# Kernel optimization log

Measured on AMD Instinct MI355X. Metric: run time of the kernel, lower is better.

## Reference

```python
import jax, jax.numpy as jnp
import numpy as np

N_NODES = 20000
N_EDGES = 50000
IN_DIM = 128
HID = 128
OUT_DIM = 64
N_PAIRS = 128
N_LAYERS = 2
N_HEADS = 4


def setup_inputs() -> dict:
    key = jax.random.key(0)
    ks = jax.random.split(key, 32)
    s = 0.05
    def p(k, shape):
        return jax.random.normal(k, shape, jnp.float32) * s
    inp = {}
    inp["node_features"] = jax.random.normal(ks[0], (N_NODES, IN_DIM), jnp.float32)
    inp["edge_index"] = jax.random.randint(ks[1], (2, N_EDGES), 0, N_NODES, jnp.int32)
    inp["edge_timestamps"] = jax.random.uniform(ks[2], (N_EDGES,), jnp.float32)
    inp["target_pairs"] = jax.random.randint(ks[3], (N_PAIRS, 2), 0, N_NODES, jnp.int32)
    inp["in_W"] = p(ks[4], (HID, IN_DIM)); inp["in_b"] = p(ks[5], (HID,))
    inp["te_W1"] = p(ks[6], (N_LAYERS, HID, 1)); inp["te_b1"] = p(ks[7], (N_LAYERS, HID))
    inp["te_W2"] = p(ks[8], (N_LAYERS, HID, HID)); inp["te_b2"] = p(ks[9], (N_LAYERS, HID))
    inp["attn_in_W"] = p(ks[10], (N_LAYERS, 3 * HID, HID)); inp["attn_in_b"] = p(ks[11], (N_LAYERS, 3 * HID))
    inp["attn_out_W"] = p(ks[12], (N_LAYERS, HID, HID)); inp["attn_out_b"] = p(ks[13], (N_LAYERS, HID))
    inp["ft_W"] = p(ks[14], (N_LAYERS, HID, HID)); inp["ft_b"] = p(ks[15], (N_LAYERS, HID))
    inp["op_W"] = p(ks[16], (N_LAYERS, HID, HID)); inp["op_b"] = p(ks[17], (N_LAYERS, HID))
    inp["out1_W"] = p(ks[18], (HID, HID)); inp["out1_b"] = p(ks[19], (HID,))
    inp["out2_W"] = p(ks[20], (OUT_DIM, HID)); inp["out2_b"] = p(ks[21], (OUT_DIM,))
    inp["lp1_W"] = p(ks[22], (HID, 2 * OUT_DIM)); inp["lp1_b"] = p(ks[23], (HID,))
    inp["lp2_W"] = p(ks[24], (HID // 2, HID)); inp["lp2_b"] = p(ks[25], (HID // 2,))
    inp["lp3_W"] = p(ks[26], (1, HID // 2)); inp["lp3_b"] = p(ks[27], (1,))
    return inp


def _forward(node_features, edge_index, edge_timestamps, target_pairs,
             in_W, in_b, te_W1, te_b1, te_W2, te_b2,
             attn_in_W, attn_in_b, attn_out_W, attn_out_b,
             ft_W, ft_b, op_W, op_b,
             out1_W, out1_b, out2_W, out2_b,
             lp1_W, lp1_b, lp2_W, lp2_b, lp3_W, lp3_b):
    N = node_features.shape[0]
    h = in_W.shape[0]
    H = N_HEADS
    d = h // H
    scale = 1.0 / np.sqrt(d).astype(np.float32)
    src, dst = edge_index[0], edge_index[1]
    # flattened target nodes; duplicates compute identical rows so dedup (torch.unique) is unneeded
    targets = target_pairs.reshape(-1)  # [U]
    U = targets.shape[0]
    E = src.shape[0]

    x = node_features @ in_W.T + in_b  # [N, h]
    for l in range(te_W1.shape[0]):
        tf = x @ ft_W[l].T + ft_b[l]                                           # [N, h]
        tfeat = jax.nn.relu(edge_timestamps[:, None] @ te_W1[l].T + te_b1[l])
        tfeat = tfeat @ te_W2[l].T + te_b2[l]                                  # [E, h]
        Wq, Wk, Wv = jnp.split(attn_in_W[l], 3, axis=0)
        bq, bk, bv = jnp.split(attn_in_b[l], 3)
        q = (tf[targets] @ Wq.T + bq).reshape(U, H, d)
        # keys/values are linear in (tf[nbr] + tfeat): split into node term A and edge term B
        Ak = (tf @ Wk.T).reshape(N, H, d)
        Bk = (tfeat @ Wk.T + bk).reshape(E, H, d)
        Av = (tf @ Wv.T).reshape(N, H, d)
        Bv = (tfeat @ Wv.T + bv).reshape(E, H, d)
        is_src = src[None, :] == targets[:, None]          # [U, E]
        mask = is_src | (dst[None, :] == targets[:, None])  # edge incident to target
        nbr = jnp.where(is_src, dst[None, :], src[None, :])  # other endpoint, [U, E]
        qAk = jnp.einsum('uhd,nhd->uhn', q, Ak) * scale      # [U, H, N]
        idx = jnp.broadcast_to(nbr[:, None, :], (U, H, E))
        s_node = jnp.take_along_axis(qAk, idx, axis=2)        # [U, H, E]
        s_edge = jnp.einsum('uhd,ehd->uhe', q, Bk) * scale
        scores = jnp.where(mask[:, None, :], s_node + s_edge, -1e30)
        p = jax.nn.softmax(scores, axis=-1)
        p = jnp.where(mask[:, None, :], p, 0.0)               # [U, H, E]
        out_edge = jnp.einsum('uhe,ehd->uhd', p, Bv)
        # sum_e p * Av[nbr] via per-target scatter of probs into node space
        w = jax.vmap(lambda pe, ne: jax.ops.segment_sum(pe, ne, num_segments=N))(
            p.transpose(0, 2, 1), nbr)                        # [U, N, H]
        out_node = jnp.einsum('unh,nhd->uhd', w, Av)
        attn = (out_node + out_edge).reshape(U, h) @ attn_out_W[l].T + attn_out_b[l]
        has_nbr = mask.any(axis=1)
        agg_in = jnp.where(has_nbr[:, None], attn, tf[targets])
        agg = agg_in @ op_W[l].T + op_b[l]
        x = x.at[targets].set(agg)
        x = jax.nn.relu(x)
    emb = jax.nn.relu(x @ out1_W.T + out1_b) @ out2_W.T + out2_b  # [N, out]
    pair = jnp.concatenate([emb[target_pairs[:, 0]], emb[target_pairs[:, 1]]], axis=1)
    z = jax.nn.relu(pair @ lp1_W.T + lp1_b)
    z = jax.nn.relu(z @ lp2_W.T + lp2_b)
    return jax.nn.sigmoid(z @ lp3_W.T + lp3_b)  # [B, 1]


def reference(node_features, edge_index, edge_timestamps, target_pairs,
              in_W, in_b, te_W1, te_b1, te_W2, te_b2,
              attn_in_W, attn_in_b, attn_out_W, attn_out_b,
              ft_W, ft_b, op_W, op_b,
              out1_W, out1_b, out2_W, out2_b,
              lp1_W, lp1_b, lp2_W, lp2_b, lp3_W, lp3_b):
    return _forward(node_features, edge_index, edge_timestamps, target_pairs,
                    in_W, in_b, te_W1, te_b1, te_W2, te_b2,
                    attn_in_W, attn_in_b, attn_out_W, attn_out_b,
                    ft_W, ft_b, op_W, op_b,
                    out1_W, out1_b, out2_W, out2_b,
                    lp1_W, lp1_b, lp2_W, lp2_b, lp3_W, lp3_b)
```

## Files before the change

kernel.cpp:

```cpp
#include <hip/hip_runtime.h>
#include <math.h>

#define N_NODES 20000
#define N_EDGES 50000
#define N_SLOTS 256
#define N_PAIRS 128
#define CAP 64
#define MSTRIDE 16384
#define NMAT 19
#define TFLAG (1 << 30)

__device__ __forceinline__ float4 relu4(float4 v) {
    return make_float4(fmaxf(v.x, 0.f), fmaxf(v.y, 0.f), fmaxf(v.z, 0.f), fmaxf(v.w, 0.f));
}
__device__ __forceinline__ float4 add4(float4 a, float4 b) {
    return make_float4(a.x + b.x, a.y + b.y, a.z + b.z, a.w + b.w);
}
__device__ __forceinline__ void fma4(float4& acc, const float4 w, const float s) {
    acc.x = fmaf(w.x, s, acc.x); acc.y = fmaf(w.y, s, acc.y);
    acc.z = fmaf(w.z, s, acc.z); acc.w = fmaf(w.w, s, acc.w);
}
#define F4Z make_float4(0.f, 0.f, 0.f, 0.f)

__device__ __forceinline__ float4 mv_ks1_g8(const float* __restrict__ WT,
                                            const float* __restrict__ xv128,
                                            int g, int jj) {
    const float4* W4 = (const float4*)WT;
    const float4* x4 = (const float4*)xv128;
    float4 acc = F4Z;
#pragma unroll
    for (int kk4 = 0; kk4 < 4; ++kk4) {
        int k4 = g * 4 + kk4;
        float4 xv = x4[k4];
        fma4(acc, W4[(k4 * 4 + 0) * 32 + jj], xv.x);
        fma4(acc, W4[(k4 * 4 + 1) * 32 + jj], xv.y);
        fma4(acc, W4[(k4 * 4 + 2) * 32 + jj], xv.z);
        fma4(acc, W4[(k4 * 4 + 3) * 32 + jj], xv.w);
    }
    return acc;
}
__device__ __forceinline__ float4 mv_ks1_g8_64(const float* __restrict__ WT,
                                               const float* __restrict__ xv128,
                                               int g, int jj) {
    const float4* W4 = (const float4*)WT;
    const float4* x4 = (const float4*)xv128;
    int j16 = jj & 15;
    float4 acc = F4Z;
#pragma unroll
    for (int kk4 = 0; kk4 < 4; ++kk4) {
        int k4 = g * 4 + kk4;
        float4 xv = x4[k4];
        fma4(acc, W4[(k4 * 4 + 0) * 16 + j16], xv.x);
        fma4(acc, W4[(k4 * 4 + 1) * 16 + j16], xv.y);
        fma4(acc, W4[(k4 * 4 + 2) * 16 + j16], xv.z);
        fma4(acc, W4[(k4 * 4 + 3) * 16 + j16], xv.w);
    }
    return acc;
}
__device__ __forceinline__ void mv8_g8(const float* __restrict__ WT,
                                       const float* __restrict__ xs,
                                       int g, int jj, float4* acc) {
    const float4* W4 = (const float4*)WT;
    const float4* x4 = (const float4*)xs;
#pragma unroll
    for (int kk4 = 0; kk4 < 4; ++kk4) {
        int k4 = g * 4 + kk4;
        float4 w0 = W4[(k4 * 4 + 0) * 32 + jj];
        float4 w1 = W4[(k4 * 4 + 1) * 32 + jj];
        float4 w2 = W4[(k4 * 4 + 2) * 32 + jj];
        float4 w3 = W4[(k4 * 4 + 3) * 32 + jj];
#pragma unroll
        for (int e = 0; e < 8; ++e) {
            float4 xv = x4[e * 32 + k4];
            fma4(acc[e], w0, xv.x); fma4(acc[e], w1, xv.y);
            fma4(acc[e], w2, xv.z); fma4(acc[e], w3, xv.w);
        }
    }
}
__device__ __forceinline__ float4 comb1_g8(const float4* pb, int jj) {
    float4 s = pb[jj];
#pragma unroll
    for (int gp = 1; gp < 8; ++gp) s = add4(s, pb[gp * 32 + jj]);
    return s;
}
__device__ __forceinline__ float4 comb8_g8(const float4* pb, int it, int jj) {
    float4 s = pb[it * 32 + jj];
#pragma unroll
    for (int gp = 1; gp < 8; ++gp) s = add4(s, pb[(gp * 8 + it) * 32 + jj]);
    return s;
}

__device__ __forceinline__ float4 mv_ks1(const float* __restrict__ WT,
                                         const float* __restrict__ xv128,
                                         int g, int jj) {
    const float4* W4 = (const float4*)WT;
    const float4* x4 = (const float4*)xv128;
    float4 acc = F4Z;
#pragma unroll 2
    for (int kk4 = 0; kk4 < 8; ++kk4) {
        int k4 = g * 8 + kk4;
        float4 xv = x4[k4];
        fma4(acc, W4[(k4 * 4 + 0) * 32 + jj], xv.x);
        fma4(acc, W4[(k4 * 4 + 1) * 32 + jj], xv.y);
        fma4(acc, W4[(k4 * 4 + 2) * 32 + jj], xv.z);
        fma4(acc, W4[(k4 * 4 + 3) * 32 + jj], xv.w);
    }
    return acc;
}
__device__ __forceinline__ float4 mv_ks1_64(const float* __restrict__ WT,
                                            const float* __restrict__ xv128,
                                            int g, int jj) {
    const float4* W4 = (const float4*)WT;
    const float4* x4 = (const float4*)xv128;
    int j16 = jj & 15;
    float4 acc = F4Z;
#pragma unroll 2
    for (int kk4 = 0; kk4 < 8; ++kk4) {
        int k4 = g * 8 + kk4;
        float4 xv = x4[k4];
        fma4(acc, W4[(k4 * 4 + 0) * 16 + j16], xv.x);
        fma4(acc, W4[(k4 * 4 + 1) * 16 + j16], xv.y);
        fma4(acc, W4[(k4 * 4 + 2) * 16 + j16], xv.z);
        fma4(acc, W4[(k4 * 4 + 3) * 16 + j16], xv.w);
    }
    return acc;
}
__device__ __forceinline__ float4 comb1(const float4* pb, int jj) {
    return add4(add4(pb[jj], pb[32 + jj]), add4(pb[64 + jj], pb[96 + jj]));
}


__global__ __launch_bounds__(256) void k_prep_tr(
    const int* __restrict__ ei, const int* __restrict__ tp,
    const float* __restrict__ inW, const float* __restrict__ ftW,
    const float* __restrict__ teW2, const float* __restrict__ aiW,
    const float* __restrict__ aoW, const float* __restrict__ opW,
    const float* __restrict__ o1W, const float* __restrict__ o2W,
    const float* __restrict__ l1W, const float* __restrict__ l2W,
    float* __restrict__ WT, int* __restrict__ cnt, int2* __restrict__ lst) {
    __shared__ float tile[32][129];
    __shared__ int tps[N_SLOTS];
    __shared__ int lc;
    const int b = blockIdx.x;
    if (threadIdx.x == 0) lc = 0;
    if (b < 72) {
        int m, r0, rows;
        if (b < 68) { m = b >> 2; r0 = (b & 3) * 32; rows = 128; }
        else { int mm = b - 68; m = 17 + (mm >> 1); r0 = (mm & 1) * 32; rows = 64; }
        const float* src;
        if (m == 0) src = inW;
        else if (m <= 2) src = ftW + (m - 1) * MSTRIDE;
        else if (m <= 4) src = teW2 + (m - 3) * MSTRIDE;
        else if (m <= 10) src = aiW + (m - 5) * MSTRIDE;
        else if (m <= 12) src = aoW + (m - 11) * MSTRIDE;
        else if (m <= 14) src = opW + (m - 13) * MSTRIDE;
        else if (m == 15) src = o1W;
        else if (m == 16) src = l1W;
        else if (m == 17) src = o2W;
        else src = l2W;
        float* dst = WT + m * MSTRIDE;
        for (int idx = threadIdx.x; idx < 32 * 128; idx += 256) {
            int r = idx >> 7, c = idx & 127;
            tile[r][c] = src[(r0 + r) * 128 + c];
        }
        __syncthreads();
        for (int idx = threadIdx.x; idx < 128 * 32; idx += 256) {
            int k = idx >> 5, jr = idx & 31;
            dst[k * rows + r0 + jr] = tile[jr][k];
        }
    }
    for (int i = threadIdx.x; i < N_SLOTS; i += 256) tps[i] = tp[i];
    __syncthreads();
    const int u = tps[b];
    const int4* src4 = (const int4*)ei;
    const int4* dst4 = (const int4*)(ei + N_EDGES);
    for (int e4 = threadIdx.x; e4 < N_EDGES / 4; e4 += 256) {
        int4 s = src4[e4];
        int4 d = dst4[e4];
        int ss[4] = {s.x, s.y, s.z, s.w};
        int dd[4] = {d.x, d.y, d.z, d.w};
#pragma unroll
        for (int t = 0; t < 4; ++t) {
            if (ss[t] == u || dd[t] == u) {
                int nbr = (ss[t] == u) ? dd[t] : ss[t];
                int pos = atomicAdd(&lc, 1);
                if (pos < CAP) lst[b * CAP + pos] = make_int2(e4 * 4 + t, nbr);
            }
        }
    }
    __syncthreads();
    if (threadIdx.x == 0) cnt[b] = lc;
    int c = min(lc, CAP);
    if (threadIdx.x < c) {
        int2 en = lst[b * CAP + threadIdx.x];
        bool ist = false;
        for (int t = 0; t < N_SLOTS; ++t) ist |= (tps[t] == en.y);
        if (ist) { en.y |= TFLAG; lst[b * CAP + threadIdx.x] = en; }
    }
}

__global__ __launch_bounds__(256) void k_layer(
    const float* __restrict__ nf, const float* __restrict__ x,
    const float* __restrict__ ts, const int* __restrict__ tp,
    const int* __restrict__ cnt, const int2* __restrict__ lst,
    const float* __restrict__ WT_in, const float* __restrict__ inb,
    const float* __restrict__ WT_ft, const float* __restrict__ ftb,
    const float* __restrict__ teW1, const float* __restrict__ teb1,
    const float* __restrict__ WT_te2, const float* __restrict__ teb2,
    const float* __restrict__ WT_q, const float* __restrict__ bq,
    const float* __restrict__ WT_k, const float* __restrict__ bk,
    const float* __restrict__ WT_v, const float* __restrict__ bv,
    const float* __restrict__ WT_ao, const float* __restrict__ aob,
    const float* __restrict__ WT_op, const float* __restrict__ opb,
    const float* __restrict__ WT_o1, const float* __restrict__ o1b,
    const float* __restrict__ WT_o2, const float* __restrict__ o2b,
    float* __restrict__ x_out, float* __restrict__ emb, int layer) {
    __shared__ __align__(16) float xu[128], x0u[128], tfv[128], qv[128], sv[128];
    __shared__ __align__(16) float xs[8 * 128], t1s[8 * 128], x0s[8 * 128], zs[8 * 128];
    __shared__ __align__(16) float4 pb[8 * 8 * 32];
    __shared__ __align__(16) float vbl[CAP * 128];
    __shared__ float scl[CAP * 4];
    __shared__ int nbr_s[8], tf_s[8];
    __shared__ float ts_s[8];
    const int slot = blockIdx.x, tid = threadIdx.x, g = tid >> 5, jj = tid & 31;
    const float scale = 0.17677669529663687f;
    const int u = tp[slot];
    const int c = min(cnt[slot], CAP);

    if (tid < 128) xu[tid] = (layer == 0) ? nf[(size_t)u * 128 + tid]
                                          : x[(size_t)u * 128 + tid];
    __syncthreads();
    const float* xeff = xu;
    if (layer == 0) {
        pb[g * 32 + jj] = mv_ks1_g8(WT_in, xu, g, jj);
        __syncthreads();
        if (g == 0)
            *(float4*)(x0u + jj * 4) = add4(comb1_g8(pb, jj), *(const float4*)(inb + jj * 4));
        xeff = x0u;
        __syncthreads();
    }
    pb[g * 32 + jj] = mv_ks1_g8(WT_ft, xeff, g, jj);
    __syncthreads();
    if (g == 0)
        *(float4*)(tfv + jj * 4) = add4(comb1_g8(pb, jj), *(const float4*)(ftb + jj * 4));
    __syncthreads();
    pb[g * 32 + jj] = mv_ks1_g8(WT_q, tfv, g, jj);
    __syncthreads();
    if (g == 0)
        *(float4*)(qv + jj * 4) = add4(comb1_g8(pb, jj), *(const float4*)(bq + jj * 4));
    __syncthreads();

    for (int base = 0; base < c; base += 8) {
        if (tid < 8) {
            int i = base + tid;
            int2 en = (i < c) ? lst[slot * CAP + i] : make_int2(0, 0);
            nbr_s[tid] = en.y & ~TFLAG;
            tf_s[tid] = (en.y & TFLAG) ? 1 : 0;
            ts_s[tid] = (i < c) ? ts[en.x] : 0.f;
        }
        __syncthreads();
        {
            int e = tid >> 5, c0 = jj * 4;
            const float* srcp = (layer == 0) ? (nf + (size_t)nbr_s[e] * 128 + c0)
                                             : (x + (size_t)nbr_s[e] * 128 + c0);
            float4 v = *(const float4*)srcp;
            float* dstp = (layer == 0) ? xs : x0s;
            *(float4*)(dstp + e * 128 + c0) = v;
            float tse = ts_s[e];
            float4 w = *(const float4*)(teW1 + c0);
            float4 b = *(const float4*)(teb1 + c0);
            *(float4*)(t1s + e * 128 + c0) =
                make_float4(fmaxf(fmaf(tse, w.x, b.x), 0.f),
                            fmaxf(fmaf(tse, w.y, b.y), 0.f),
                            fmaxf(fmaf(tse, w.z, b.z), 0.f),
                            fmaxf(fmaf(tse, w.w, b.w), 0.f));
        }
        __syncthreads();
        if (layer == 0) {
            float4 acc[8] = {F4Z, F4Z, F4Z, F4Z, F4Z, F4Z, F4Z, F4Z};
            mv8_g8(WT_in, xs, g, jj, acc);
#pragma unroll
            for (int e = 0; e < 8; ++e) pb[(g * 8 + e) * 32 + jj] = acc[e];
            __syncthreads();
            {
                float4 x0v = add4(comb8_g8(pb, g, jj), *(const float4*)(inb + jj * 4));
                *(float4*)(x0s + g * 128 + jj * 4) = x0v;
                if (base + g < c && !tf_s[g])
                    *(float4*)(x_out + (size_t)nbr_s[g] * 128 + jj * 4) = relu4(x0v);
            }
            __syncthreads();
        }
        {
            float4 acc[8] = {F4Z, F4Z, F4Z, F4Z, F4Z, F4Z, F4Z, F4Z};
            mv8_g8(WT_ft, x0s, g, jj, acc);
#pragma unroll
            for (int e = 0; e < 8; ++e) pb[(g * 8 + e) * 32 + jj] = acc[e];
            __syncthreads();
            float4 za = comb8_g8(pb, g, jj);
            __syncthreads();
            float4 acc2[8] = {F4Z, F4Z, F4Z, F4Z, F4Z, F4Z, F4Z, F4Z};
            mv8_g8(WT_te2, t1s, g, jj, acc2);
#pragma unroll
            for (int e = 0; e < 8; ++e) pb[(g * 8 + e) * 32 + jj] = acc2[e];
            __syncthreads();
            float4 zb = comb8_g8(pb, g, jj);
            float4 z4 = add4(add4(za, zb),
                             add4(*(const float4*)(ftb + jj * 4),
                                  *(const float4*)(teb2 + jj * 4)));
            *(float4*)(zs + g * 128 + jj * 4) = z4;
            __syncthreads();
        }
        {
            float4 acc[8] = {F4Z, F4Z, F4Z, F4Z, F4Z, F4Z, F4Z, F4Z};
            mv8_g8(WT_k, zs, g, jj, acc);
#pragma unroll
            for (int e = 0; e < 8; ++e) pb[(g * 8 + e) * 32 + jj] = acc[e];
            __syncthreads();
            float4 kk = add4(comb8_g8(pb, g, jj), *(const float4*)(bk + jj * 4));
            __syncthreads();
            float4 acc2[8] = {F4Z, F4Z, F4Z, F4Z, F4Z, F4Z, F4Z, F4Z};
            mv8_g8(WT_v, zs, g, jj, acc2);
#pragma unroll
            for (int e = 0; e < 8; ++e) pb[(g * 8 + e) * 32 + jj] = acc2[e];
            __syncthreads();
            float4 vv = add4(comb8_g8(pb, g, jj), *(const float4*)(bv + jj * 4));
            float4 q4 = *(const float4*)(qv + jj * 4);
            float pr = q4.x * kk.x + q4.y * kk.y + q4.z * kk.z + q4.w * kk.w;
            pr += __shfl_xor(pr, 1);
            pr += __shfl_xor(pr, 2);
            pr += __shfl_xor(pr, 4);
            if (base + g < c) {
                if ((jj & 7) == 0) scl[(base + g) * 4 + (jj >> 3)] = pr * scale;
                *(float4*)(vbl + (base + g) * 128 + jj * 4) = vv;
            }
            __syncthreads();
        }
    }

    if (tid < 128) {
        int h = tid >> 5;
        if (c > 0) {
            float m = -INFINITY;
            for (int i = 0; i < c; ++i) m = fmaxf(m, scl[i * 4 + h]);
            float l = 0.f, o = 0.f;
            for (int i = 0; i < c; ++i) {
                float p = __expf(scl[i * 4 + h] - m);
                l += p;
                o = fmaf(p, vbl[i * 128 + tid], o);
            }
            sv[tid] = o / l;
        } else {
            sv[tid] = 0.f;
        }
    }
    __syncthreads();
    pb[g * 32 + jj] = mv_ks1_g8(WT_ao, sv, g, jj);
    __syncthreads();
    if (g == 0) {
        float4 z4;
        if (c > 0) z4 = add4(comb1_g8(pb, jj), *(const float4*)(aob + jj * 4));
        else z4 = *(const float4*)(tfv + jj * 4);
        *(float4*)(xu + jj * 4) = z4;
    }
    __syncthreads();
    pb[g * 32 + jj] = mv_ks1_g8(WT_op, xu, g, jj);
    __syncthreads();
    if (layer == 0) {
        if (g == 0) {
            float4 a = relu4(add4(comb1_g8(pb, jj), *(const float4*)(opb + jj * 4)));
            *(float4*)(x_out + (size_t)u * 128 + jj * 4) = a;
        }
        return;
    }
    if (g == 0)
        *(float4*)(x0u + jj * 4) =
            relu4(add4(comb1_g8(pb, jj), *(const float4*)(opb + jj * 4)));
    __syncthreads();
    pb[g * 32 + jj] = mv_ks1_g8(WT_o1, x0u, g, jj);
    __syncthreads();
    if (g == 0)
        *(float4*)(tfv + jj * 4) =
            relu4(add4(comb1_g8(pb, jj), *(const float4*)(o1b + jj * 4)));
    __syncthreads();
    pb[g * 32 + jj] = mv_ks1_g8_64(WT_o2, tfv, g, jj);
    __syncthreads();
    if (g == 0 && jj < 16)
        *(float4*)(emb + (size_t)slot * 64 + jj * 4) =
            add4(comb1_g8(pb, jj), *(const float4*)(o2b + jj * 4));
}

__global__ __launch_bounds__(128) void k_pair(
    const float* __restrict__ emb,
    const float* __restrict__ WT_l1, const float* __restrict__ l1b,
    const float* __restrict__ WT_l2, const float* __restrict__ l2b,
    const float* __restrict__ l3W, const float* __restrict__ l3b,
    float* __restrict__ out) {
    __shared__ __align__(16) float pv[128], z1[128], z2s[64];
    __shared__ __align__(16) float4 pb[4 * 32];
    const int p = blockIdx.x, tid = threadIdx.x, g = tid >> 5, jj = tid & 31;
    pv[tid] = (tid < 64) ? emb[(size_t)(2 * p) * 64 + tid]
                         : emb[(size_t)(2 * p + 1) * 64 + (tid - 64)];
    __syncthreads();
    pb[g * 32 + jj] = mv_ks1(WT_l1, pv, g, jj);
    __syncthreads();
    if (g == 0)
        *(float4*)(z1 + jj * 4) = relu4(add4(comb1(pb, jj), *(const float4*)(l1b + jj * 4)));
    __syncthreads();
    pb[g * 32 + jj] = mv_ks1_64(WT_l2, z1, g, jj);
    __syncthreads();
    if (g == 0 && jj < 16)
        *(float4*)(z2s + jj * 4) = relu4(add4(comb1(pb, jj), *(const float4*)(l2b + jj * 4)));
    __syncthreads();
    if (tid < 64) {
        float v = z2s[tid] * l3W[tid];
        v += __shfl_xor(v, 1);
        v += __shfl_xor(v, 2);
        v += __shfl_xor(v, 4);
        v += __shfl_xor(v, 8);
        v += __shfl_xor(v, 16);
        v += __shfl_xor(v, 32);
        if (tid == 0) out[p] = 1.f / (1.f + __expf(-(v + l3b[0])));
    }
}

extern "C" void kernel_launch(void* const* d_in, const int* in_sizes, int n_in,
                              void* d_out, int out_size, void* d_ws, size_t ws_size,
                              hipStream_t stream) {
    const float* nf  = (const float*)d_in[0];
    const int*   ei  = (const int*)d_in[1];
    const float* ts  = (const float*)d_in[2];
    const int*   tp  = (const int*)d_in[3];
    const float* inW = (const float*)d_in[4];
    const float* inb = (const float*)d_in[5];
    const float* teW1 = (const float*)d_in[6];
    const float* teb1 = (const float*)d_in[7];
    const float* teW2 = (const float*)d_in[8];
    const float* teb2 = (const float*)d_in[9];
    const float* aiW = (const float*)d_in[10];
    const float* aib = (const float*)d_in[11];
    const float* aoW = (const float*)d_in[12];
    const float* aob = (const float*)d_in[13];
    const float* ftW = (const float*)d_in[14];
    const float* ftb = (const float*)d_in[15];
    const float* opW = (const float*)d_in[16];
    const float* opb = (const float*)d_in[17];
    const float* o1W = (const float*)d_in[18];
    const float* o1b = (const float*)d_in[19];
    const float* o2W = (const float*)d_in[20];
    const float* o2b = (const float*)d_in[21];
    const float* l1W = (const float*)d_in[22];
    const float* l1b = (const float*)d_in[23];
    const float* l2W = (const float*)d_in[24];
    const float* l2b = (const float*)d_in[25];
    const float* l3W = (const float*)d_in[26];
    const float* l3b = (const float*)d_in[27];
    float* out = (float*)d_out;

    char* ws = (char*)d_ws;
    size_t off = 0;
    float* x    = (float*)(ws + off); off += (size_t)N_NODES * 128 * 4;
    int*   cnt  = (int*)  (ws + off); off += N_SLOTS * 4;
    int2*  lst  = (int2*) (ws + off); off += (size_t)N_SLOTS * CAP * 8;
    float* emb  = (float*)(ws + off); off += N_SLOTS * 64 * 4;
    float* WT   = (float*)(ws + off); off += (size_t)NMAT * MSTRIDE * 4;

    k_prep_tr<<<N_SLOTS, 256, 0, stream>>>(ei, tp, inW, ftW, teW2, aiW, aoW, opW,
                                           o1W, o2W, l1W, l2W, WT, cnt, lst);

    for (int l = 0; l < 2; ++l) {
        const float* WT_ft = WT + (1 + l) * MSTRIDE;
        const float* WT_te2 = WT + (3 + l) * MSTRIDE;
        const float* WT_q = WT + (5 + 3 * l) * MSTRIDE;
        const float* WT_k = WT + (6 + 3 * l) * MSTRIDE;
        const float* WT_v = WT + (7 + 3 * l) * MSTRIDE;
        const float* WT_ao = WT + (11 + l) * MSTRIDE;
        const float* WT_op = WT + (13 + l) * MSTRIDE;
        const float* bq = aib + l * 384;
        k_layer<<<N_SLOTS, 256, 0, stream>>>(
            nf, x, ts, tp, cnt, lst,
            WT, inb, WT_ft, ftb + l * 128, teW1 + l * 128, teb1 + l * 128,
            WT_te2, teb2 + l * 128, WT_q, bq, WT_k, bq + 128, WT_v, bq + 256,
            WT_ao, aob + l * 128, WT_op, opb + l * 128,
            WT + 15 * MSTRIDE, o1b, WT + 17 * MSTRIDE, o2b,
            x, emb, l);
    }
    k_pair<<<N_PAIRS, 128, 0, stream>>>(emb, WT + 16 * MSTRIDE, l1b,
                                        WT + 18 * MSTRIDE, l2b, l3W, l3b, out);
}
```

Measured before the change: 203.9 us.

## Fuse all stages into one persistent kernel with grid barriers and hashed edge scan

Merges the prep, two layer kernels and the pair-predictor into a single persistent kernel of 256 blocks that sync through atomic-counter grid barriers. This removes several launch gaps. Edge-list construction changes from every block scanning all 50000 edges for its own target to one block scanning the edges once against a shared-memory hash of target nodes. That block appends entries to per-slot lists with atomics, which puts the whole edge scan on a single block's critical path before the first barrier. The approach also relies on all 256 blocks being co-resident and adds a memset launch for the barrier counter.

```diff
diff --git a/kernel.cpp b/kernel.cpp
--- a/kernel.cpp
+++ b/kernel.cpp
@@ -9,6 +9,8 @@
 #define MSTRIDE 16384
 #define NMAT 19
 #define TFLAG (1 << 30)
+#define HSZ 1024
+#define NBLK 256
 
 __device__ __forceinline__ float4 relu4(float4 v) {
     return make_float4(fmaxf(v.x, 0.f), fmaxf(v.y, 0.f), fmaxf(v.z, 0.f), fmaxf(v.w, 0.f));
@@ -21,6 +23,18 @@
     acc.z = fmaf(w.z, s, acc.z); acc.w = fmaf(w.w, s, acc.w);
 }
 #define F4Z make_float4(0.f, 0.f, 0.f, 0.f)
+
+__device__ __forceinline__ void gbar(unsigned* cnt, unsigned target) {
+    __syncthreads();
+    if (threadIdx.x == 0) {
+        __threadfence();
+        __hip_atomic_fetch_add(cnt, 1u, __ATOMIC_ACQ_REL, __HIP_MEMORY_SCOPE_AGENT);
+        while (__hip_atomic_load(cnt, __ATOMIC_ACQUIRE, __HIP_MEMORY_SCOPE_AGENT) < target)
+            __builtin_amdgcn_s_sleep(1);
+        __threadfence();
+    }
+    __syncthreads();
+}
 
 __device__ __forceinline__ float4 mv_ks1_g8(const float* __restrict__ WT,
                                             const float* __restrict__ xv128,
@@ -129,92 +143,49 @@
     return add4(add4(pb[jj], pb[32 + jj]), add4(pb[64 + jj], pb[96 + jj]));
 }
 
-
-__global__ __launch_bounds__(256) void k_prep_tr(
-    const int* __restrict__ ei, const int* __restrict__ tp,
-    const float* __restrict__ inW, const float* __restrict__ ftW,
-    const float* __restrict__ teW2, const float* __restrict__ aiW,
-    const float* __restrict__ aoW, const float* __restrict__ opW,
-    const float* __restrict__ o1W, const float* __restrict__ o2W,
-    const float* __restrict__ l1W, const float* __restrict__ l2W,
-    float* __restrict__ WT, int* __restrict__ cnt, int2* __restrict__ lst) {
-    __shared__ float tile[32][129];
-    __shared__ int tps[N_SLOTS];
-    __shared__ int lc;
-    const int b = blockIdx.x;
-    if (threadIdx.x == 0) lc = 0;
-    if (b < 72) {
-        int m, r0, rows;
-        if (b < 68) { m = b >> 2; r0 = (b & 3) * 32; rows = 128; }
-        else { int mm = b - 68; m = 17 + (mm >> 1); r0 = (mm & 1) * 32; rows = 64; }
-        const float* src;
-        if (m == 0) src = inW;
-        else if (m <= 2) src = ftW + (m - 1) * MSTRIDE;
-        else if (m <= 4) src = teW2 + (m - 3) * MSTRIDE;
-        else if (m <= 10) src = aiW + (m - 5) * MSTRIDE;
-        else if (m <= 12) src = aoW + (m - 11) * MSTRIDE;
-        else if (m <= 14) src = opW + (m - 13) * MSTRIDE;
-        else if (m == 15) src = o1W;
-        else if (m == 16) src = l1W;
-        else if (m == 17) src = o2W;
-        else src = l2W;
-        float* dst = WT + m * MSTRIDE;
-        for (int idx = threadIdx.x; idx < 32 * 128; idx += 256) {
-            int r = idx >> 7, c = idx & 127;
-            tile[r][c] = src[(r0 + r) * 128 + c];
-        }
-        __syncthreads();
-        for (int idx = threadIdx.x; idx < 128 * 32; idx += 256) {
-            int k = idx >> 5, jr = idx & 31;
-            dst[k * rows + r0 + jr] = tile[jr][k];
-        }
-    }
-    for (int i = threadIdx.x; i < N_SLOTS; i += 256) tps[i] = tp[i];
-    __syncthreads();
-    const int u = tps[b];
-    const int4* src4 = (const int4*)ei;
-    const int4* dst4 = (const int4*)(ei + N_EDGES);
-    for (int e4 = threadIdx.x; e4 < N_EDGES / 4; e4 += 256) {
-        int4 s = src4[e4];
-        int4 d = dst4[e4];
-        int ss[4] = {s.x, s.y, s.z, s.w};
-        int dd[4] = {d.x, d.y, d.z, d.w};
-#pragma unroll
-        for (int t = 0; t < 4; ++t) {
-            if (ss[t] == u || dd[t] == u) {
-                int nbr = (ss[t] == u) ? dd[t] : ss[t];
-                int pos = atomicAdd(&lc, 1);
-                if (pos < CAP) lst[b * CAP + pos] = make_int2(e4 * 4 + t, nbr);
-            }
-        }
-    }
-    __syncthreads();
-    if (threadIdx.x == 0) cnt[b] = lc;
-    int c = min(lc, CAP);
-    if (threadIdx.x < c) {
-        int2 en = lst[b * CAP + threadIdx.x];
-        bool ist = false;
-        for (int t = 0; t < N_SLOTS; ++t) ist |= (tps[t] == en.y);
-        if (ist) { en.y |= TFLAG; lst[b * CAP + threadIdx.x] = en; }
-    }
-}
-
-__global__ __launch_bounds__(256) void k_layer(
-    const float* __restrict__ nf, const float* __restrict__ x,
-    const float* __restrict__ ts, const int* __restrict__ tp,
-    const int* __restrict__ cnt, const int2* __restrict__ lst,
-    const float* __restrict__ WT_in, const float* __restrict__ inb,
-    const float* __restrict__ WT_ft, const float* __restrict__ ftb,
-    const float* __restrict__ teW1, const float* __restrict__ teb1,
-    const float* __restrict__ WT_te2, const float* __restrict__ teb2,
-    const float* __restrict__ WT_q, const float* __restrict__ bq,
-    const float* __restrict__ WT_k, const float* __restrict__ bk,
-    const float* __restrict__ WT_v, const float* __restrict__ bv,
-    const float* __restrict__ WT_ao, const float* __restrict__ aob,
-    const float* __restrict__ WT_op, const float* __restrict__ opb,
-    const float* __restrict__ WT_o1, const float* __restrict__ o1b,
-    const float* __restrict__ WT_o2, const float* __restrict__ o2b,
-    float* __restrict__ x_out, float* __restrict__ emb, int layer) {
+__device__ __forceinline__ unsigned thash(int key) {
+    return ((unsigned)key * 2654435761u) >> 22;
+}
+__device__ __forceinline__ bool hexists(const int* __restrict__ hkey, int key) {
+    unsigned h = thash(key);
+    while (true) {
+        int k = hkey[h];
+        if (k == -1) return false;
+        if (k == key) return true;
+        h = (h + 1) & (HSZ - 1);
+    }
+}
+__device__ __forceinline__ void hemit(const int* __restrict__ hkey,
+                                      const int* __restrict__ hval,
+                                      int* lcnt, int2* __restrict__ lst,
+                                      int key, int e, int nbrf) {
+    unsigned h = thash(key);
+    while (true) {
+        int k = hkey[h];
+        if (k == -1) return;
+        if (k == key) {
+            int s = hval[h];
+            int pos = atomicAdd(&lcnt[s], 1);
+            if (pos < CAP) lst[s * CAP + pos] = make_int2(e, nbrf);
+        }
+        h = (h + 1) & (HSZ - 1);
+    }
+}
+
+struct Params {
+    const float* nf; const int* ei; const float* ts; const int* tp;
+    const float* inW; const float* inb;
+    const float* teW1; const float* teb1; const float* teW2; const float* teb2;
+    const float* aiW; const float* aib; const float* aoW; const float* aob;
+    const float* ftW; const float* ftb; const float* opW; const float* opb;
+    const float* o1W; const float* o1b; const float* o2W; const float* o2b;
+    const float* l1W; const float* l1b; const float* l2W; const float* l2b;
+    const float* l3W; const float* l3b;
+    float* out; float* x; int* cnt; int2* lst; float* emb; float* WT;
+    unsigned* bar;
+};
+
+__global__ __launch_bounds__(256, 1) void k_fused(Params P) {
     __shared__ __align__(16) float xu[128], x0u[128], tfv[128], qv[128], sv[128];
     __shared__ __align__(16) float xs[8 * 128], t1s[8 * 128], x0s[8 * 128], zs[8 * 128];
     __shared__ __align__(16) float4 pb[8 * 8 * 32];
@@ -222,268 +193,333 @@
     __shared__ float scl[CAP * 4];
     __shared__ int nbr_s[8], tf_s[8];
     __shared__ float ts_s[8];
-    const int slot = blockIdx.x, tid = threadIdx.x, g = tid >> 5, jj = tid & 31;
+    __shared__ __align__(16) float tile[32][129];
+    __shared__ int hkey[HSZ], hval[HSZ];
+    __shared__ int lcnt[N_SLOTS];
+
+    const int b = blockIdx.x, tid = threadIdx.x, g = tid >> 5, jj = tid & 31;
+
+    if (b < 72) {
+        int m, r0, rows;
+        if (b < 68) { m = b >> 2; r0 = (b & 3) * 32; rows = 128; }
+        else { int mm = b - 68; m = 17 + (mm >> 1); r0 = (mm & 1) * 32; rows = 64; }
+        const float* src;
+        if (m == 0) src = P.inW;
+        else if (m <= 2) src = P.ftW + (m - 1) * MSTRIDE;
+        else if (m <= 4) src = P.teW2 + (m - 3) * MSTRIDE;
+        else if (m <= 10) src = P.aiW + (m - 5) * MSTRIDE;
+        else if (m <= 12) src = P.aoW + (m - 11) * MSTRIDE;
+        else if (m <= 14) src = P.opW + (m - 13) * MSTRIDE;
+        else if (m == 15) src = P.o1W;
+        else if (m == 16) src = P.l1W;
+        else if (m == 17) src = P.o2W;
+        else src = P.l2W;
+        float* dst = P.WT + m * MSTRIDE;
+        for (int idx = tid; idx < 32 * 128; idx += 256) {
+            int r = idx >> 7, cc = idx & 127;
+            tile[r][cc] = src[(r0 + r) * 128 + cc];
+        }
+        __syncthreads();
+        for (int idx = tid; idx < 128 * 32; idx += 256) {
+            int k = idx >> 5, jr = idx & 31;
+            dst[k * rows + r0 + jr] = tile[jr][k];
+        }
+    } else if (b == 72) {
+        for (int i = tid; i < HSZ; i += 256) hkey[i] = -1;
+        lcnt[tid] = 0;
+        __syncthreads();
+        {
+            int uu = P.tp[tid];
+            unsigned h = thash(uu);
+            while (atomicCAS(&hkey[h], -1, uu) != -1) h = (h + 1) & (HSZ - 1);
+            hval[h] = tid;
+        }
+        __syncthreads();
+        const int4* s4 = (const int4*)P.ei;
+        const int4* d4 = (const int4*)(P.ei + N_EDGES);
+        for (int e4 = tid; e4 < N_EDGES / 4; e4 += 256) {
+            int4 s = s4[e4];
+            int4 d = d4[e4];
+            int ss[4] = {s.x, s.y, s.z, s.w};
+            int dd[4] = {d.x, d.y, d.z, d.w};
+#pragma unroll
+            for (int t = 0; t < 4; ++t) {
+                int a = ss[t], bb = dd[t];
+                bool atgt = hexists(hkey, a);
+                bool btgt = (bb == a) ? atgt : hexists(hkey, bb);
+                if (!atgt && !btgt) continue;
+                int e = e4 * 4 + t;
+                if (atgt) hemit(hkey, hval, lcnt, P.lst, a, e, bb | (btgt ? TFLAG : 0));
+                if (btgt && bb != a) hemit(hkey, hval, lcnt, P.lst, bb, e, a | (atgt ? TFLAG : 0));
+            }
+        }
+        __syncthreads();
+        P.cnt[tid] = lcnt[tid];
+    }
+    gbar(P.bar, NBLK);
+
     const float scale = 0.17677669529663687f;
-    const int u = tp[slot];
-    const int c = min(cnt[slot], CAP);
-
-    if (tid < 128) xu[tid] = (layer == 0) ? nf[(size_t)u * 128 + tid]
-                                          : x[(size_t)u * 128 + tid];
-    __syncthreads();
-    const float* xeff = xu;
-    if (layer == 0) {
-        pb[g * 32 + jj] = mv_ks1_g8(WT_in, xu, g, jj);
+    const int u = P.tp[b];
+    const int c = min(P.cnt[b], CAP);
+
+    for (int layer = 0; layer < 2; ++layer) {
+        const float* WT_in = P.WT;
+        const float* WT_ft = P.WT + (1 + layer) * MSTRIDE;
+        const float* WT_te2 = P.WT + (3 + layer) * MSTRIDE;
+        const float* WT_q = P.WT + (5 + 3 * layer) * MSTRIDE;
+        const float* WT_k = P.WT + (6 + 3 * layer) * MSTRIDE;
+        const float* WT_v = P.WT + (7 + 3 * layer) * MSTRIDE;
+        const float* WT_ao = P.WT + (11 + layer) * MSTRIDE;
+        const float* WT_op = P.WT + (13 + layer) * MSTRIDE;
+        const float* inb = P.inb;
+        const float* ftb = P.ftb + layer * 128;
+        const float* teW1 = P.teW1 + layer * 128;
+        const float* teb1 = P.teb1 + layer * 128;
+        const float* teb2 = P.teb2 + layer * 128;
+        const float* bq = P.aib + layer * 384;
+        const float* bk = bq + 128;
+        const float* bv = bq + 256;
+        const float* aob = P.aob + layer * 128;
+        const float* opb = P.opb + layer * 128;
+
+        if (tid < 128) xu[tid] = (layer == 0) ? P.nf[(size_t)u * 128 + tid]
+                                              : P.x[(size_t)u * 128 + tid];
+        __syncthreads();
+        const float* xeff = xu;
+        if (layer == 0) {
+            pb[g * 32 + jj] = mv_ks1_g8(WT_in, xu, g, jj);
+            __syncthreads();
+            if (g == 0)
+                *(float4*)(x0u + jj * 4) = add4(comb1_g8(pb, jj), *(const float4*)(inb + jj * 4));
+            xeff = x0u;
+            __syncthreads();
+        }
+        pb[g * 32 + jj] = mv_ks1_g8(WT_ft, xeff, g, jj);
         __syncthreads();
         if (g == 0)
-            *(float4*)(x0u + jj * 4) = add4(comb1_g8(pb, jj), *(const float4*)(inb + jj * 4));
-        xeff = x0u;
-        __syncthreads();
-    }
-    pb[g * 32 + jj] = mv_ks1_g8(WT_ft, xeff, g, jj);
-    __syncthreads();
-    if (g == 0)
-        *(float4*)(tfv + jj * 4) = add4(comb1_g8(pb, jj), *(const float4*)(ftb + jj * 4));
-    __syncthreads();
-    pb[g * 32 + jj] = mv_ks1_g8(WT_q, tfv, g, jj);
-    __syncthreads();
-    if (g == 0)
-        *(float4*)(qv + jj * 4) = add4(comb1_g8(pb, jj), *(const float4*)(bq + jj * 4));
-    __syncthreads();
-
-    for (int base = 0; base < c; base += 8) {
-        if (tid < 8) {
-            int i = base + tid;
-            int2 en = (i < c) ? lst[slot * CAP + i] : make_int2(0, 0);
-            nbr_s[tid] = en.y & ~TFLAG;
-            tf_s[tid] = (en.y & TFLAG) ? 1 : 0;
-            ts_s[tid] = (i < c) ? ts[en.x] : 0.f;
-        }
-        __syncthreads();
-        {
-            int e = tid >> 5, c0 = jj * 4;
-            const float* srcp = (layer == 0) ? (nf + (size_t)nbr_s[e] * 128 + c0)
-                                             : (x + (size_t)nbr_s[e] * 128 + c0);
-            float4 v = *(const float4*)srcp;
-            float* dstp = (layer == 0) ? xs : x0s;
-            *(float4*)(dstp + e * 128 + c0) = v;
-            float tse = ts_s[e];
-            float4 w = *(const float4*)(teW1 + c0);
-            float4 b = *(const float4*)(teb1 + c0);
-            *(float4*)(t1s + e * 128 + c0) =
-                make_float4(fmaxf(fmaf(tse, w.x, b.x), 0.f),
-                            fmaxf(fmaf(tse, w.y, b.y), 0.f),
-                            fmaxf(fmaf(tse, w.z, b.z), 0.f),
-                            fmaxf(fmaf(tse, w.w, b.w), 0.f));
-        }
+            *(float4*)(tfv + jj * 4) = add4(comb1_g8(pb, jj), *(const float4*)(ftb + jj * 4));
+        __syncthreads();
+        pb[g * 32 + jj] = mv_ks1_g8(WT_q, tfv, g, jj);
+        __syncthreads();
+        if (g == 0)
+            *(float4*)(qv + jj * 4) = add4(comb1_g8(pb, jj), *(const float4*)(bq + jj * 4));
+        __syncthreads();
+
+        for (int base = 0; base < c; base += 8) {
+            if (tid < 8) {
+                int i = base + tid;
+                int2 en = (i < c) ? P.lst[b * CAP + i] : make_int2(0, 0);
+                nbr_s[tid] = en.y & ~TFLAG;
+                tf_s[tid] = (en.y & TFLAG) ? 1 : 0;
+                ts_s[tid] = (i < c) ? P.ts[en.x] : 0.f;
+            }
+            __syncthreads();
+            {
+                int e = tid >> 5, c0 = jj * 4;
+                const float* srcp = (layer == 0) ? (P.nf + (size_t)nbr_s[e] * 128 + c0)
+                                                 : (P.x + (size_t)nbr_s[e] * 128 + c0);
+                float4 v = *(const float4*)srcp;
+                float* dstp = (layer == 0) ? xs : x0s;
+                *(float4*)(dstp + e * 128 + c0) = v;
+                float tse = ts_s[e];
+                float4 w = *(const float4*)(teW1 + c0);
+                float4 bb = *(const float4*)(teb1 + c0);
+                *(float4*)(t1s + e * 128 + c0) =
+                    make_float4(fmaxf(fmaf(tse, w.x, bb.x), 0.f),
+                                fmaxf(fmaf(tse, w.y, bb.y), 0.f),
+                                fmaxf(fmaf(tse, w.z, bb.z), 0.f),
+                                fmaxf(fmaf(tse, w.w, bb.w), 0.f));
+            }
+            __syncthreads();
+            if (layer == 0) {
+                float4 acc[8] = {F4Z, F4Z, F4Z, F4Z, F4Z, F4Z, F4Z, F4Z};
+                mv8_g8(WT_in, xs, g, jj, acc);
+#pragma unroll
+                for (int e = 0; e < 8; ++e) pb[(g * 8 + e) * 32 + jj] = acc[e];
+                __syncthreads();
+                {
+                    float4 x0v = add4(comb8_g8(pb, g, jj), *(const float4*)(inb + jj * 4));
+                    *(float4*)(x0s + g * 128 + jj * 4) = x0v;
+                    if (base + g < c && !tf_s[g])
+                        *(float4*)(P.x + (size_t)nbr_s[g] * 128 + jj * 4) = relu4(x0v);
+                }
+                __syncthreads();
+            }
+            {
+                float4 acc[8] = {F4Z, F4Z, F4Z, F4Z, F4Z, F4Z, F4Z, F4Z};
+                mv8_g8(WT_ft, x0s, g, jj, acc);
+#pragma unroll
+                for (int e = 0; e < 8; ++e) pb[(g * 8 + e) * 32 + jj] = acc[e];
+                __syncthreads();
+                float4 za = comb8_g8(pb, g, jj);
+                __syncthreads();
+                float4 acc2[8] = {F4Z, F4Z, F4Z, F4Z, F4Z, F4Z, F4Z, F4Z};
+                mv8_g8(WT_te2, t1s, g, jj, acc2);
+#pragma unroll
+                for (int e = 0; e < 8; ++e) pb[(g * 8 + e) * 32 + jj] = acc2[e];
+                __syncthreads();
+                float4 zb = comb8_g8(pb, g, jj);
+                float4 z4 = add4(add4(za, zb),
+                                 add4(*(const float4*)(ftb + jj * 4),
+                                      *(const float4*)(teb2 + jj * 4)));
+                *(float4*)(zs + g * 128 + jj * 4) = z4;
+                __syncthreads();
+            }
+            {
+                float4 acc[8] = {F4Z, F4Z, F4Z, F4Z, F4Z, F4Z, F4Z, F4Z};
+                mv8_g8(WT_k, zs, g, jj, acc);
+#pragma unroll
+                for (int e = 0; e < 8; ++e) pb[(g * 8 + e) * 32 + jj] = acc[e];
+                __syncthreads();
+                float4 kk = add4(comb8_g8(pb, g, jj), *(const float4*)(bk + jj * 4));
+                __syncthreads();
+                float4 acc2[8] = {F4Z, F4Z, F4Z, F4Z, F4Z, F4Z, F4Z, F4Z};
+                mv8_g8(WT_v, zs, g, jj, acc2);
+#pragma unroll
+                for (int e = 0; e < 8; ++e) pb[(g * 8 + e) * 32 + jj] = acc2[e];
+                __syncthreads();
+                float4 vv = add4(comb8_g8(pb, g, jj), *(const float4*)(bv + jj * 4));
+                float4 q4 = *(const float4*)(qv + jj * 4);
+                float pr = q4.x * kk.x + q4.y * kk.y + q4.z * kk.z + q4.w * kk.w;
+                pr += __shfl_xor(pr, 1);
+                pr += __shfl_xor(pr, 2);
+                pr += __shfl_xor(pr, 4);
+                if (base + g < c) {
+                    if ((jj & 7) == 0) scl[(base + g) * 4 + (jj >> 3)] = pr * scale;
+                    *(float4*)(vbl + (base + g) * 128 + jj * 4) = vv;
+                }
+                __syncthreads();
+            }
+        }
+
+        if (tid < 128) {
+            int h = tid >> 5;
+            if (c > 0) {
+                float m = -INFINITY;
+                for (int i = 0; i < c; ++i) m = fmaxf(m, scl[i * 4 + h]);
+                float l = 0.f, o = 0.f;
+                for (int i = 0; i < c; ++i) {
+                    float p = __expf(scl[i * 4 + h] - m);
+                    l += p;
+                    o = fmaf(p, vbl[i * 128 + tid], o);
+                }
+                sv[tid] = o / l;
+            } else {
+                sv[tid] = 0.f;
+            }
+        }
+        __syncthreads();
+        pb[g * 32 + jj] = mv_ks1_g8(WT_ao, sv, g, jj);
+        __syncthreads();
+        if (g == 0) {
+            float4 z4;
+            if (c > 0) z4 = add4(comb1_g8(pb, jj), *(const float4*)(aob + jj * 4));
+            else z4 = *(const float4*)(tfv + jj * 4);
+            *(float4*)(xu + jj * 4) = z4;
+        }
+        __syncthreads();
+        pb[g * 32 + jj] = mv_ks1_g8(WT_op, xu, g, jj);
         __syncthreads();
         if (layer == 0) {
-            float4 acc[8] = {F4Z, F4Z, F4Z, F4Z, F4Z, F4Z, F4Z, F4Z};
-            mv8_g8(WT_in, xs, g, jj, acc);
-#pragma unroll
-            for (int e = 0; e < 8; ++e) pb[(g * 8 + e) * 32 + jj] = acc[e];
-            __syncthreads();
-            {
-                float4 x0v = add4(comb8_g8(pb, g, jj), *(const float4*)(inb + jj * 4));
-                *(float4*)(x0s + g * 128 + jj * 4) = x0v;
-                if (base + g < c && !tf_s[g])
-                    *(float4*)(x_out + (size_t)nbr_s[g] * 128 + jj * 4) = relu4(x0v);
-            }
-            __syncthreads();
-        }
-        {
-            float4 acc[8] = {F4Z, F4Z, F4Z, F4Z, F4Z, F4Z, F4Z, F4Z};
-            mv8_g8(WT_ft, x0s, g, jj, acc);
-#pragma unroll
-            for (int e = 0; e < 8; ++e) pb[(g * 8 + e) * 32 + jj] = acc[e];
-            __syncthreads();
-            float4 za = comb8_g8(pb, g, jj);
-            __syncthreads();
-            float4 acc2[8] = {F4Z, F4Z, F4Z, F4Z, F4Z, F4Z, F4Z, F4Z};
-            mv8_g8(WT_te2, t1s, g, jj, acc2);
-#pragma unroll
-            for (int e = 0; e < 8; ++e) pb[(g * 8 + e) * 32 + jj] = acc2[e];
-            __syncthreads();
-            float4 zb = comb8_g8(pb, g, jj);
-            float4 z4 = add4(add4(za, zb),
-                             add4(*(const float4*)(ftb + jj * 4),
-                                  *(const float4*)(teb2 + jj * 4)));
-            *(float4*)(zs + g * 128 + jj * 4) = z4;
-            __syncthreads();
-        }
-        {
-            float4 acc[8] = {F4Z, F4Z, F4Z, F4Z, F4Z, F4Z, F4Z, F4Z};
-            mv8_g8(WT_k, zs, g, jj, acc);
-#pragma unroll
-            for (int e = 0; e < 8; ++e) pb[(g * 8 + e) * 32 + jj] = acc[e];
-            __syncthreads();
-            float4 kk = add4(comb8_g8(pb, g, jj), *(const float4*)(bk + jj * 4));
-            __syncthreads();
-            float4 acc2[8] = {F4Z, F4Z, F4Z, F4Z, F4Z, F4Z, F4Z, F4Z};
-            mv8_g8(WT_v, zs, g, jj, acc2);
-#pragma unroll
-            for (int e = 0; e < 8; ++e) pb[(g * 8 + e) * 32 + jj] = acc2[e];
-            __syncthreads();
-            float4 vv = add4(comb8_g8(pb, g, jj), *(const float4*)(bv + jj * 4));
-            float4 q4 = *(const float4*)(qv + jj * 4);
-            float pr = q4.x * kk.x + q4.y * kk.y + q4.z * kk.z + q4.w * kk.w;
-            pr += __shfl_xor(pr, 1);
-            pr += __shfl_xor(pr, 2);
-            pr += __shfl_xor(pr, 4);
-            if (base + g < c) {
-                if ((jj & 7) == 0) scl[(base + g) * 4 + (jj >> 3)] = pr * scale;
-                *(float4*)(vbl + (base + g) * 128 + jj * 4) = vv;
-            }
-            __syncthreads();
-        }
-    }
-
-    if (tid < 128) {
-        int h = tid >> 5;
-        if (c > 0) {
-            float m = -INFINITY;
-            for (int i = 0; i < c; ++i) m = fmaxf(m, scl[i * 4 + h]);
-            float l = 0.f, o = 0.f;
-            for (int i = 0; i < c; ++i) {
-                float p = __expf(scl[i * 4 + h] - m);
-                l += p;
-                o = fmaf(p, vbl[i * 128 + tid], o);
-            }
-            sv[tid] = o / l;
+            if (g == 0) {
+                float4 a = relu4(add4(comb1_g8(pb, jj), *(const float4*)(opb + jj * 4)));
+                *(float4*)(P.x + (size_t)u * 128 + jj * 4) = a;
+            }
         } else {
-            sv[tid] = 0.f;
-        }
-    }
-    __syncthreads();
-    pb[g * 32 + jj] = mv_ks1_g8(WT_ao, sv, g, jj);
-    __syncthreads();
-    if (g == 0) {
-        float4 z4;
-        if (c > 0) z4 = add4(comb1_g8(pb, jj), *(const float4*)(aob + jj * 4));
-        else z4 = *(const float4*)(tfv + jj * 4);
-        *(float4*)(xu + jj * 4) = z4;
-    }
-    __syncthreads();
-    pb[g * 32 + jj] = mv_ks1_g8(WT_op, xu, g, jj);
-    __syncthreads();
-    if (layer == 0) {
-        if (g == 0) {
-            float4 a = relu4(add4(comb1_g8(pb, jj), *(const float4*)(opb + jj * 4)));
-            *(float4*)(x_out + (size_t)u * 128 + jj * 4) = a;
-        }
-        return;
-    }
-    if (g == 0)
-        *(float4*)(x0u + jj * 4) =
-            relu4(add4(comb1_g8(pb, jj), *(const float4*)(opb + jj * 4)));
-    __syncthreads();
-    pb[g * 32 + jj] = mv_ks1_g8(WT_o1, x0u, g, jj);
-    __syncthreads();
-    if (g == 0)
-        *(float4*)(tfv + jj * 4) =
-            relu4(add4(comb1_g8(pb, jj), *(const float4*)(o1b + jj * 4)));
-    __syncthreads();
-    pb[g * 32 + jj] = mv_ks1_g8_64(WT_o2, tfv, g, jj);
-    __syncthreads();
-    if (g == 0 && jj < 16)
-        *(float4*)(emb + (size_t)slot * 64 + jj * 4) =
-            add4(comb1_g8(pb, jj), *(const float4*)(o2b + jj * 4));
-}
-
-__global__ __launch_bounds__(128) void k_pair(
-    const float* __restrict__ emb,
-    const float* __restrict__ WT_l1, const float* __restrict__ l1b,
-    const float* __restrict__ WT_l2, const float* __restrict__ l2b,
-    const float* __restrict__ l3W, const float* __restrict__ l3b,
-    float* __restrict__ out) {
-    __shared__ __align__(16) float pv[128], z1[128], z2s[64];
-    __shared__ __align__(16) float4 pb[4 * 32];
-    const int p = blockIdx.x, tid = threadIdx.x, g = tid >> 5, jj = tid & 31;
-    pv[tid] = (tid < 64) ? emb[(size_t)(2 * p) * 64 + tid]
-                         : emb[(size_t)(2 * p + 1) * 64 + (tid - 64)];
-    __syncthreads();
-    pb[g * 32 + jj] = mv_ks1(WT_l1, pv, g, jj);
-    __syncthreads();
-    if (g == 0)
-        *(float4*)(z1 + jj * 4) = relu4(add4(comb1(pb, jj), *(const float4*)(l1b + jj * 4)));
-    __syncthreads();
-    pb[g * 32 + jj] = mv_ks1_64(WT_l2, z1, g, jj);
-    __syncthreads();
-    if (g == 0 && jj < 16)
-        *(float4*)(z2s + jj * 4) = relu4(add4(comb1(pb, jj), *(const float4*)(l2b + jj * 4)));
-    __syncthreads();
-    if (tid < 64) {
-        float v = z2s[tid] * l3W[tid];
-        v += __shfl_xor(v, 1);
-        v += __shfl_xor(v, 2);
-        v += __shfl_xor(v, 4);
-        v += __shfl_xor(v, 8);
-        v += __shfl_xor(v, 16);
-        v += __shfl_xor(v, 32);
-        if (tid == 0) out[p] = 1.f / (1.f + __expf(-(v + l3b[0])));
+            if (g == 0)
+                *(float4*)(x0u + jj * 4) =
+                    relu4(add4(comb1_g8(pb, jj), *(const float4*)(opb + jj * 4)));
+            __syncthreads();
+            pb[g * 32 + jj] = mv_ks1_g8(P.WT + 15 * MSTRIDE, x0u, g, jj);
+            __syncthreads();
+            if (g == 0)
+                *(float4*)(tfv + jj * 4) =
+                    relu4(add4(comb1_g8(pb, jj), *(const float4*)(P.o1b + jj * 4)));
+            __syncthreads();
+            pb[g * 32 + jj] = mv_ks1_g8_64(P.WT + 17 * MSTRIDE, tfv, g, jj);
+            __syncthreads();
+            if (g == 0 && jj < 16)
+                *(float4*)(P.emb + (size_t)b * 64 + jj * 4) =
+                    add4(comb1_g8(pb, jj), *(const float4*)(P.o2b + jj * 4));
+        }
+        gbar(P.bar, NBLK * (2 + layer));
+    }
+
+    if (b < N_PAIRS) {
+        const float* WT_l1 = P.WT + 16 * MSTRIDE;
+        const float* WT_l2 = P.WT + 18 * MSTRIDE;
+        if (tid < 128)
+            xu[tid] = (tid < 64) ? P.emb[(size_t)(2 * b) * 64 + tid]
+                                 : P.emb[(size_t)(2 * b + 1) * 64 + (tid - 64)];
+        __syncthreads();
+        if (tid < 128) pb[g * 32 + jj] = mv_ks1(WT_l1, xu, g, jj);
+        __syncthreads();
+        if (tid < 128 && g == 0)
+            *(float4*)(tfv + jj * 4) =
+                relu4(add4(comb1(pb, jj), *(const float4*)(P.l1b + jj * 4)));
+        __syncthreads();
+        if (tid < 128) pb[g * 32 + jj] = mv_ks1_64(WT_l2, tfv, g, jj);
+        __syncthreads();
+        if (tid < 128 && g == 0 && jj < 16)
+            *(float4*)(qv + jj * 4) =
+                relu4(add4(comb1(pb, jj), *(const float4*)(P.l2b + jj * 4)));
+        __syncthreads();
+        if (tid < 64) {
+            float v = qv[tid] * P.l3W[tid];
+            v += __shfl_xor(v, 1);
+            v += __shfl_xor(v, 2);
+            v += __shfl_xor(v, 4);
+            v += __shfl_xor(v, 8);
+            v += __shfl_xor(v, 16);
+            v += __shfl_xor(v, 32);
+            if (tid == 0) P.out[b] = 1.f / (1.f + __expf(-(v + P.l3b[0])));
+        }
     }
 }
 
 extern "C" void kernel_launch(void* const* d_in, const int* in_sizes, int n_in,
                               void* d_out, int out_size, void* d_ws, size_t ws_size,
                               hipStream_t stream) {
-    const float* nf  = (const float*)d_in[0];
-    const int*   ei  = (const int*)d_in[1];
-    const float* ts  = (const float*)d_in[2];
-    const int*   tp  = (const int*)d_in[3];
-    const float* inW = (const float*)d_in[4];
-    const float* inb = (const float*)d_in[5];
-    const float* teW1 = (const float*)d_in[6];
-    const float* teb1 = (const float*)d_in[7];
-    const float* teW2 = (const float*)d_in[8];
-    const float* teb2 = (const float*)d_in[9];
-    const float* aiW = (const float*)d_in[10];
-    const float* aib = (const float*)d_in[11];
-    const float* aoW = (const float*)d_in[12];
-    const float* aob = (const float*)d_in[13];
-    const float* ftW = (const float*)d_in[14];
-    const float* ftb = (const float*)d_in[15];
-    const float* opW = (const float*)d_in[16];
-    const float* opb = (const float*)d_in[17];
-    const float* o1W = (const float*)d_in[18];
-    const float* o1b = (const float*)d_in[19];
-    const float* o2W = (const float*)d_in[20];
-    const float* o2b = (const float*)d_in[21];
-    const float* l1W = (const float*)d_in[22];
-    const float* l1b = (const float*)d_in[23];
-    const float* l2W = (const float*)d_in[24];
-    const float* l2b = (const float*)d_in[25];
-    const float* l3W = (const float*)d_in[26];
-    const float* l3b = (const float*)d_in[27];
-    float* out = (float*)d_out;
+    Params P;
+    P.nf  = (const float*)d_in[0];
+    P.ei  = (const int*)d_in[1];
+    P.ts  = (const float*)d_in[2];
+    P.tp  = (const int*)d_in[3];
+    P.inW = (const float*)d_in[4];
+    P.inb = (const float*)d_in[5];
+    P.teW1 = (const float*)d_in[6];
+    P.teb1 = (const float*)d_in[7];
+    P.teW2 = (const float*)d_in[8];
+    P.teb2 = (const float*)d_in[9];
+    P.aiW = (const float*)d_in[10];
+    P.aib = (const float*)d_in[11];
+    P.aoW = (const float*)d_in[12];
+    P.aob = (const float*)d_in[13];
+    P.ftW = (const float*)d_in[14];
+    P.ftb = (const float*)d_in[15];
+    P.opW = (const float*)d_in[16];
+    P.opb = (const float*)d_in[17];
+    P.o1W = (const float*)d_in[18];
+    P.o1b = (const float*)d_in[19];
+    P.o2W = (const float*)d_in[20];
+    P.o2b = (const float*)d_in[21];
+    P.l1W = (const float*)d_in[22];
+    P.l1b = (const float*)d_in[23];
+    P.l2W = (const float*)d_in[24];
+    P.l2b = (const float*)d_in[25];
+    P.l3W = (const float*)d_in[26];
+    P.l3b = (const float*)d_in[27];
+    P.out = (float*)d_out;
 
     char* ws = (char*)d_ws;
     size_t off = 0;
-    float* x    = (float*)(ws + off); off += (size_t)N_NODES * 128 * 4;
-    int*   cnt  = (int*)  (ws + off); off += N_SLOTS * 4;
-    int2*  lst  = (int2*) (ws + off); off += (size_t)N_SLOTS * CAP * 8;
-    float* emb  = (float*)(ws + off); off += N_SLOTS * 64 * 4;
-    float* WT   = (float*)(ws + off); off += (size_t)NMAT * MSTRIDE * 4;
-
-    k_prep_tr<<<N_SLOTS, 256, 0, stream>>>(ei, tp, inW, ftW, teW2, aiW, aoW, opW,
-                                           o1W, o2W, l1W, l2W, WT, cnt, lst);
-
-    for (int l = 0; l < 2; ++l) {
-        const float* WT_ft = WT + (1 + l) * MSTRIDE;
-        const float* WT_te2 = WT + (3 + l) * MSTRIDE;
-        const float* WT_q = WT + (5 + 3 * l) * MSTRIDE;
-        const float* WT_k = WT + (6 + 3 * l) * MSTRIDE;
-        const float* WT_v = WT + (7 + 3 * l) * MSTRIDE;
-        const float* WT_ao = WT + (11 + l) * MSTRIDE;
-        const float* WT_op = WT + (13 + l) * MSTRIDE;
-        const float* bq = aib + l * 384;
-        k_layer<<<N_SLOTS, 256, 0, stream>>>(
-            nf, x, ts, tp, cnt, lst,
-            WT, inb, WT_ft, ftb + l * 128, teW1 + l * 128, teb1 + l * 128,
-            WT_te2, teb2 + l * 128, WT_q, bq, WT_k, bq + 128, WT_v, bq + 256,
-            WT_ao, aob + l * 128, WT_op, opb + l * 128,
-            WT + 15 * MSTRIDE, o1b, WT + 17 * MSTRIDE, o2b,
-            x, emb, l);
-    }
-    k_pair<<<N_PAIRS, 128, 0, stream>>>(emb, WT + 16 * MSTRIDE, l1b,
-                                        WT + 18 * MSTRIDE, l2b, l3W, l3b, out);
-}
+    P.x    = (float*)(ws + off); off += (size_t)N_NODES * 128 * 4;
+    P.cnt  = (int*)  (ws + off); off += N_SLOTS * 4;
+    P.lst  = (int2*) (ws + off); off += (size_t)N_SLOTS * CAP * 8;
+    P.emb  = (float*)(ws + off); off += N_SLOTS * 64 * 4;
+    P.WT   = (float*)(ws + off); off += (size_t)NMAT * MSTRIDE * 4;
+    P.bar  = (unsigned*)(ws + off); off += 256;
+
+    hipMemsetAsync(P.bar, 0, 4, stream);
+    k_fused<<<NBLK, 256, 0, stream>>>(P);
+}
```

Measured after the change: 676.5 us. +231.8%, slower.
